# Performance work log

Hardware: AMD Instinct MI355X
Metric: run time of the kernel (lower is better)

The kernel has to match this reference:

```python
import jax, jax.numpy as jnp
import numpy as np

B, S, D = 512, 8, 1024
L = 6        # n_layers
LOOPS = 4    # n_loops
EPS = 1e-5   # LayerNorm eps (torch default)


def setup_inputs() -> dict:
    key = jax.random.key(0)
    ks = jax.random.split(key, 8)
    s = 1.0 / np.sqrt(D)  # torch Linear default init bound
    x = jax.random.normal(ks[0], (B, S, D), jnp.float32)
    gamma = jnp.ones((L, D), jnp.float32)
    beta = jnp.zeros((L, D), jnp.float32)
    Wg = jax.random.uniform(ks[1], (L, D, D), jnp.float32, -s, s)
    bg = jax.random.uniform(ks[2], (L, D), jnp.float32, -s, s)
    Wt = jax.random.uniform(ks[3], (L, D, D), jnp.float32, -s, s)
    bt = jax.random.uniform(ks[4], (L, D), jnp.float32, -s, s)
    Wc = jax.random.uniform(ks[5], (D, 1), jnp.float32, -s, s)
    bc = jax.random.uniform(ks[6], (1,), jnp.float32, -s, s)
    return {"x": x, "gamma": gamma, "beta": beta, "Wg": Wg, "bg": bg,
            "Wt": Wt, "bt": bt, "Wc": Wc, "bc": bc}


def _block(x, gamma, beta, Wg, bg, Wt, bt):
    # LayerNorm over last dim
    mu = jnp.mean(x, axis=-1, keepdims=True)
    var = jnp.mean(jnp.square(x - mu), axis=-1, keepdims=True)
    xn = (x - mu) * jax.lax.rsqrt(var + EPS) * gamma + beta
    g = jax.nn.sigmoid(jnp.einsum('bsd,de->bse', xn, Wg) + bg)
    t = jnp.tanh(jnp.einsum('bsd,de->bse', xn, Wt) + bt)
    return x * (1.0 - g) + t * g


def reference(x, gamma, beta, Wg, bg, Wt, bt, Wc, bc):
    confs = []
    for _ in range(LOOPS):
        for i in range(L):
            x = _block(x, gamma[i], beta[i], Wg[i], bg[i], Wt[i], bt[i])
        # confidence = sigmoid(Linear(x.mean(dim=1)))  -> (B, 1)
        confs.append(jax.nn.sigmoid(x.mean(axis=1) @ Wc + bc))
    return x, jnp.stack(confs)  # ((B,S,D), (LOOPS,B,1))
```

## Files before the change

### kernel.cpp

```cpp
#include <hip/hip_runtime.h>
#include <hip/hip_bf16.h>
#include <math.h>

#define B_ 512
#define S_ 8
#define D_ 1024
#define L_ 6
#define LOOPS_ 4
#define R_ (B_*S_)
#define LD_ (L_*D_)
#define EPSV 1e-5f

#define BM 128
#define BN 64
#define BK 64
#define NT (D_/BK)
#define BUF_USH 16384

typedef __attribute__((ext_vector_type(4))) float f32x4;
typedef __attribute__((ext_vector_type(8))) _Float16 f16x8;

__device__ __forceinline__ float bf2f(unsigned short u){
  union { float f; unsigned int i; } v; v.i = ((unsigned int)u) << 16; return v.f;
}
__device__ __forceinline__ unsigned short f2h(float f){
  _Float16 h = (_Float16)f;
  union { _Float16 h; unsigned short u; } v; v.h = h; return v.u;
}
__device__ __forceinline__ float loadf(const void* p, size_t i, int bf){
  return bf ? bf2f(((const unsigned short*)p)[i]) : ((const float*)p)[i];
}
__device__ __forceinline__ void gload16(const void* g, void* l){
  __builtin_amdgcn_global_load_lds((const __attribute__((address_space(1))) void*)g,
                                   (__attribute__((address_space(3))) void*)l, 16, 0, 0);
}

__global__ void k_detect(const unsigned int* __restrict__ gamma_raw, int* __restrict__ flag){
  if (threadIdx.x == 0 && blockIdx.x == 0)
    *flag = (gamma_raw[0] == 0x3F803F80u) ? 1 : 0;
}

__global__ void k_x2f(const void* __restrict__ x, float* __restrict__ xf,
                      const int* __restrict__ flag, int n4){
  int i = blockIdx.x * blockDim.x + threadIdx.x;
  if (i >= n4) return;
  if (*flag){
    ushort4 u = ((const ushort4*)x)[i];
    float4 f; f.x = bf2f(u.x); f.y = bf2f(u.y); f.z = bf2f(u.z); f.w = bf2f(u.w);
    ((float4*)xf)[i] = f;
  } else {
    ((float4*)xf)[i] = ((const float4*)x)[i];
  }
}

__global__ void k_small(const void* g, const void* b, const void* bgp, const void* btp,
                        const void* wcp, const void* bcp,
                        float* __restrict__ sm, const int* __restrict__ flag){
  int i = blockIdx.x * blockDim.x + threadIdx.x;
  int bf = *flag;
  if (i < LD_)               sm[i] = loadf(g,   i,          bf);
  else if (i < 2*LD_)        sm[i] = loadf(b,   i - LD_,    bf);
  else if (i < 3*LD_)        sm[i] = loadf(bgp, i - 2*LD_,  bf);
  else if (i < 4*LD_)        sm[i] = loadf(btp, i - 3*LD_,  bf);
  else if (i < 4*LD_ + D_)   sm[i] = loadf(wcp, i - 4*LD_,  bf);
  else if (i == 4*LD_ + D_)  sm[i] = loadf(bcp, 0,          bf);
}

__global__ void k_transpose(const void* __restrict__ Wg, const void* __restrict__ Wt,
                            ushort* __restrict__ WgT, ushort* __restrict__ WtT,
                            const int* __restrict__ flag){
  __shared__ ushort tile[32][33];
  int bf = *flag;
  int z = blockIdx.z;
  const void* src; ushort* dst;
  size_t base;
  if (z < L_) { src = Wg; dst = WgT + (size_t)z * D_ * D_;        base = (size_t)z * D_ * D_; }
  else        { src = Wt; dst = WtT + (size_t)(z - L_) * D_ * D_; base = (size_t)(z - L_) * D_ * D_; }
  int d0 = blockIdx.y * 32, e0 = blockIdx.x * 32;
  int tx = threadIdx.x, ty = threadIdx.y;
  #pragma unroll
  for (int i = 0; i < 4; i++){
    int r = ty + i * 8;
    size_t idx = base + (size_t)(d0 + r) * D_ + e0 + tx;
    float v = bf ? bf2f(((const ushort*)src)[idx]) : ((const float*)src)[idx];
    tile[r][tx] = f2h(v);
  }
  __syncthreads();
  #pragma unroll
  for (int i = 0; i < 4; i++){
    int r = ty + i * 8;
    dst[(size_t)(e0 + r) * D_ + d0 + tx] = tile[tx][r];
  }
}

__global__ __launch_bounds__(256) void k_ln(const float* __restrict__ xf,
            const float* __restrict__ gamma, const float* __restrict__ beta,
            ushort* __restrict__ xh){
  int row = blockIdx.x;
  int t = threadIdx.x;
  const float4* xr = (const float4*)(xf + (size_t)row * D_);
  float4 v = xr[t];
  float s = v.x + v.y + v.z + v.w;
  float q = v.x * v.x + v.y * v.y + v.z * v.z + v.w * v.w;
  #pragma unroll
  for (int o = 32; o; o >>= 1){ s += __shfl_xor(s, o); q += __shfl_xor(q, o); }
  __shared__ float ss[8], qq[8];
  int w = t >> 6, lane = t & 63;
  if (lane == 0){ ss[w] = s; qq[w] = q; }
  __syncthreads();
  if (t == 0){
    float S = ss[0] + ss[1] + ss[2] + ss[3];
    float Q = qq[0] + qq[1] + qq[2] + qq[3];
    float mu = S * (1.0f / D_);
    float var = Q * (1.0f / D_) - mu * mu;
    ss[4] = mu; qq[4] = rsqrtf(var + EPSV);
  }
  __syncthreads();
  float mu = ss[4], rs = qq[4];
  float4 gm4 = ((const float4*)gamma)[t];
  float4 bb4 = ((const float4*)beta)[t];
  float xv[4] = { v.x, v.y, v.z, v.w };
  float gm[4] = { gm4.x, gm4.y, gm4.z, gm4.w };
  float bb[4] = { bb4.x, bb4.y, bb4.z, bb4.w };
  ushort hu[4];
  #pragma unroll
  for (int j = 0; j < 4; j++){
    float xn = (xv[j] - mu) * rs * gm[j] + bb[j];
    hu[j] = f2h(xn);
  }
  ushort4 ho; ho.x = hu[0]; ho.y = hu[1]; ho.z = hu[2]; ho.w = hu[3];
  ((ushort4*)(xh + (size_t)row * D_))[t] = ho;
}

__device__ __forceinline__ void stage_tile(const ushort* __restrict__ xh,
    const ushort* __restrict__ wg, const ushort* __restrict__ wt,
    ushort* __restrict__ buf, int mbase, int nbase, int kb, int w, int lane)
{
  int rr = lane >> 3;
  int clog = (lane & 7) ^ rr;
  int coff = kb + clog * 8;
  #pragma unroll
  for (int i = 0; i < 4; i++){
    int row = (w * 4 + i) * 8 + rr;
    gload16(xh + (size_t)(mbase + row) * D_ + coff, buf + (w * 4 + i) * 512);
  }
  #pragma unroll
  for (int i = 0; i < 2; i++){
    int row = (w * 2 + i) * 8 + rr;
    gload16(wg + (size_t)(nbase + row) * D_ + coff, buf + 8192 + (w * 2 + i) * 512);
    gload16(wt + (size_t)(nbase + row) * D_ + coff, buf + 12288 + (w * 2 + i) * 512);
  }
}

__global__ __launch_bounds__(256, 2) void k_gemm_gate(
    const ushort* __restrict__ xh,
    const ushort* __restrict__ WgT, const ushort* __restrict__ WtT,
    const float* __restrict__ bgf, const float* __restrict__ btf,
    float* __restrict__ xf)
{
  __shared__ __align__(16) ushort smem[2 * BUF_USH];

  int t = threadIdx.x;
  int lane = t & 63, w = t >> 6;
  int wm = w >> 1, wn = w & 1;

  int bid = blockIdx.x;
  int swz = (bid & 7) * 64 + (bid >> 3);
  int mbase = (swz >> 4) * BM;
  int nbase = (swz & 15) * BN;

  f32x4 accg[4][2], acct[4][2];
  #pragma unroll
  for (int i = 0; i < 4; i++)
    #pragma unroll
    for (int j = 0; j < 2; j++){
      accg[i][j] = (f32x4){0.f, 0.f, 0.f, 0.f};
      acct[i][j] = (f32x4){0.f, 0.f, 0.f, 0.f};
    }

  ushort* b0 = smem;
  ushort* b1 = smem + BUF_USH;

  stage_tile(xh, WgT, WtT, b0, mbase, nbase, 0, w, lane);

  for (int kt = 0; kt < NT; ++kt){
    __syncthreads();
    ushort* cb = (kt & 1) ? b1 : b0;
    ushort* nbuf = (kt & 1) ? b0 : b1;
    if (kt < NT - 1)
      stage_tile(xh, WgT, WtT, nbuf, mbase, nbase, (kt + 1) * BK, w, lane);

    const ushort* bA = cb;
    const ushort* bG = cb + 8192;
    const ushort* bT = cb + 12288;
    #pragma unroll
    for (int ks = 0; ks < 2; ks++){
      int cl = ks * 4 + (lane >> 4);
      f16x8 af[4], bg2[2], bt2[2];
      #pragma unroll
      for (int mf = 0; mf < 4; mf++){
        int r = wm * 64 + mf * 16 + (lane & 15);
        af[mf] = *(const f16x8*)(bA + r * 64 + ((cl ^ (r & 7)) << 3));
      }
      #pragma unroll
      for (int nf = 0; nf < 2; nf++){
        int r = wn * 32 + nf * 16 + (lane & 15);
        int off = r * 64 + ((cl ^ (r & 7)) << 3);
        bg2[nf] = *(const f16x8*)(bG + off);
        bt2[nf] = *(const f16x8*)(bT + off);
      }
      #pragma unroll
      for (int mf = 0; mf < 4; mf++)
        #pragma unroll
        for (int nf = 0; nf < 2; nf++){
          accg[mf][nf] = __builtin_amdgcn_mfma_f32_16x16x32_f16(af[mf], bg2[nf], accg[mf][nf], 0, 0, 0);
          acct[mf][nf] = __builtin_amdgcn_mfma_f32_16x16x32_f16(af[mf], bt2[nf], acct[mf][nf], 0, 0, 0);
        }
    }
  }

  #pragma unroll
  for (int mf = 0; mf < 4; mf++){
    int row0 = mbase + wm * 64 + mf * 16 + ((lane >> 4) * 4);
    #pragma unroll
    for (int nf = 0; nf < 2; nf++){
      int col = nbase + wn * 32 + nf * 16 + (lane & 15);
      float bgv = bgf[col];
      float btv = btf[col];
      #pragma unroll
      for (int j = 0; j < 4; j++){
        float ug = accg[mf][nf][j] + bgv;
        float ut = acct[mf][nf][j] + btv;
        float g = 1.0f / (1.0f + expf(-ug));
        float tt = tanhf(ut);
        size_t idx = (size_t)(row0 + j) * D_ + col;
        float xo = xf[idx];
        xf[idx] = xo + g * (tt - xo);
      }
    }
  }
}

__global__ __launch_bounds__(256) void k_conf(const float* __restrict__ xf, const float* __restrict__ Wc,
                       const float* __restrict__ bc, float* __restrict__ out, int loop){
  int b = blockIdx.x;
  int t = threadIdx.x;
  const float* xb = xf + (size_t)b * S_ * D_;
  float acc = 0.f;
  for (int i = t; i < S_ * D_; i += 256){
    int d = i & (D_ - 1);
    acc += xb[i] * Wc[d];
  }
  #pragma unroll
  for (int o = 32; o; o >>= 1) acc += __shfl_xor(acc, o);
  __shared__ float wsum[4];
  int w = t >> 6, lane = t & 63;
  if (lane == 0) wsum[w] = acc;
  __syncthreads();
  if (t == 0){
    float s = wsum[0] + wsum[1] + wsum[2] + wsum[3];
    float z = s * (1.0f / S_) + bc[0];
    float c = 1.0f / (1.0f + expf(-z));
    out[(size_t)R_ * D_ + (size_t)loop * B_ + b] = c;
  }
}

__global__ void k_f2x(const float* __restrict__ xf, float* __restrict__ out, int n4){
  int i = blockIdx.x * blockDim.x + threadIdx.x;
  if (i >= n4) return;
  ((float4*)out)[i] = ((const float4*)xf)[i];
}

extern "C" void kernel_launch(void* const* d_in, const int* in_sizes, int n_in,
                              void* d_out, int out_size, void* d_ws, size_t ws_size,
                              hipStream_t stream){
  const void* x     = d_in[0];
  const void* gamma = d_in[1];
  const void* beta  = d_in[2];
  const void* Wg    = d_in[3];
  const void* bg    = d_in[4];
  const void* Wt    = d_in[5];
  const void* bt    = d_in[6];
  const void* Wc    = d_in[7];
  const void* bc    = d_in[8];
  float* out = (float*)d_out;

  char* ws = (char*)d_ws;
  float*  xf  = (float*)ws;
  ushort* xh  = (ushort*)(ws + (size_t)R_ * D_ * 4);
  ushort* WgT = xh + (size_t)R_ * D_;
  ushort* WtT = WgT + (size_t)L_ * D_ * D_;
  float*  sm  = (float*)(WtT + (size_t)L_ * D_ * D_);
  int*    flag = (int*)(sm + 4 * LD_ + D_ + 1);

  k_detect<<<1, 64, 0, stream>>>((const unsigned int*)gamma, flag);
  k_x2f<<<4096, 256, 0, stream>>>(x, xf, flag, R_ * D_ / 4);
  k_small<<<(4 * LD_ + D_ + 1 + 255) / 256, 256, 0, stream>>>(gamma, beta, bg, bt, Wc, bc, sm, flag);
  dim3 tb(32, 8); dim3 tg(D_ / 32, D_ / 32, 2 * L_);
  k_transpose<<<tg, tb, 0, stream>>>(Wg, Wt, WgT, WtT, flag);

  const float* smG  = sm;
  const float* smB  = sm + LD_;
  const float* smBg = sm + 2 * LD_;
  const float* smBt = sm + 3 * LD_;
  const float* smWc = sm + 4 * LD_;
  const float* smBc = sm + 4 * LD_ + D_;

  for (int loop = 0; loop < LOOPS_; ++loop){
    for (int l = 0; l < L_; ++l){
      k_ln<<<R_, 256, 0, stream>>>(xf, smG + (size_t)l * D_, smB + (size_t)l * D_, xh);
      k_gemm_gate<<<512, 256, 0, stream>>>(xh,
                                           WgT + (size_t)l * D_ * D_, WtT + (size_t)l * D_ * D_,
                                           smBg + (size_t)l * D_, smBt + (size_t)l * D_, xf);
    }
    k_conf<<<B_, 256, 0, stream>>>(xf, smWc, smBc, out, loop);
  }
  k_f2x<<<4096, 256, 0, stream>>>(xf, out, R_ * D_ / 4);
}
```

Measured before the change: 910.5 us.

## Load GEMM A operand directly to registers and use one wave per LayerNorm row

The GEMM no longer stages the activation (A) tile through LDS. Each wave loads its A fragments straight from global memory into registers, prefetched one k-step ahead, and only the two weight tiles stay in LDS. This halves LDS use and bandwidth, but raises register pressure and makes the A loads from global less coalesced. LayerNorm now handles one row per wave with four rows per block, which removes the shared-memory reductions and barriers.

```diff
diff --git a/kernel.cpp b/kernel.cpp
--- a/kernel.cpp
+++ b/kernel.cpp
@@ -15,7 +15,7 @@
 #define BN 64
 #define BK 64
 #define NT (D_/BK)
-#define BUF_USH 16384
+#define BUF_USH 8192
 
 typedef __attribute__((ext_vector_type(4))) float f32x4;
 typedef __attribute__((ext_vector_type(8))) _Float16 f16x8;
@@ -96,60 +96,60 @@
 __global__ __launch_bounds__(256) void k_ln(const float* __restrict__ xf,
             const float* __restrict__ gamma, const float* __restrict__ beta,
             ushort* __restrict__ xh){
-  int row = blockIdx.x;
-  int t = threadIdx.x;
-  const float4* xr = (const float4*)(xf + (size_t)row * D_);
-  float4 v = xr[t];
-  float s = v.x + v.y + v.z + v.w;
-  float q = v.x * v.x + v.y * v.y + v.z * v.z + v.w * v.w;
+  int w = threadIdx.x >> 6, lane = threadIdx.x & 63;
+  int row = blockIdx.x * 4 + w;
+  const float* xr = xf + (size_t)row * D_;
+  float4 v[4];
+  float s = 0.f, q = 0.f;
+  #pragma unroll
+  for (int p = 0; p < 4; p++){
+    v[p] = *(const float4*)(xr + p * 256 + lane * 4);
+    s += v[p].x + v[p].y + v[p].z + v[p].w;
+    q += v[p].x * v[p].x + v[p].y * v[p].y + v[p].z * v[p].z + v[p].w * v[p].w;
+  }
   #pragma unroll
   for (int o = 32; o; o >>= 1){ s += __shfl_xor(s, o); q += __shfl_xor(q, o); }
-  __shared__ float ss[8], qq[8];
-  int w = t >> 6, lane = t & 63;
-  if (lane == 0){ ss[w] = s; qq[w] = q; }
-  __syncthreads();
-  if (t == 0){
-    float S = ss[0] + ss[1] + ss[2] + ss[3];
-    float Q = qq[0] + qq[1] + qq[2] + qq[3];
-    float mu = S * (1.0f / D_);
-    float var = Q * (1.0f / D_) - mu * mu;
-    ss[4] = mu; qq[4] = rsqrtf(var + EPSV);
-  }
-  __syncthreads();
-  float mu = ss[4], rs = qq[4];
-  float4 gm4 = ((const float4*)gamma)[t];
-  float4 bb4 = ((const float4*)beta)[t];
-  float xv[4] = { v.x, v.y, v.z, v.w };
-  float gm[4] = { gm4.x, gm4.y, gm4.z, gm4.w };
-  float bb[4] = { bb4.x, bb4.y, bb4.z, bb4.w };
-  ushort hu[4];
-  #pragma unroll
-  for (int j = 0; j < 4; j++){
-    float xn = (xv[j] - mu) * rs * gm[j] + bb[j];
-    hu[j] = f2h(xn);
-  }
-  ushort4 ho; ho.x = hu[0]; ho.y = hu[1]; ho.z = hu[2]; ho.w = hu[3];
-  ((ushort4*)(xh + (size_t)row * D_))[t] = ho;
-}
-
-__device__ __forceinline__ void stage_tile(const ushort* __restrict__ xh,
-    const ushort* __restrict__ wg, const ushort* __restrict__ wt,
-    ushort* __restrict__ buf, int mbase, int nbase, int kb, int w, int lane)
+  float mu = s * (1.0f / D_);
+  float var = q * (1.0f / D_) - mu * mu;
+  float rs = rsqrtf(var + EPSV);
+  #pragma unroll
+  for (int p = 0; p < 4; p++){
+    float4 g4 = *(const float4*)(gamma + p * 256 + lane * 4);
+    float4 b4 = *(const float4*)(beta  + p * 256 + lane * 4);
+    ushort4 o4;
+    o4.x = f2h((v[p].x - mu) * rs * g4.x + b4.x);
+    o4.y = f2h((v[p].y - mu) * rs * g4.y + b4.y);
+    o4.z = f2h((v[p].z - mu) * rs * g4.z + b4.z);
+    o4.w = f2h((v[p].w - mu) * rs * g4.w + b4.w);
+    *(ushort4*)(xh + (size_t)row * D_ + p * 256 + lane * 4) = o4;
+  }
+}
+
+__device__ __forceinline__ void stage_B(const ushort* __restrict__ wg,
+    const ushort* __restrict__ wt, ushort* __restrict__ buf,
+    int nbase, int kb, int w, int lane)
 {
   int rr = lane >> 3;
   int clog = (lane & 7) ^ rr;
   int coff = kb + clog * 8;
   #pragma unroll
-  for (int i = 0; i < 4; i++){
-    int row = (w * 4 + i) * 8 + rr;
-    gload16(xh + (size_t)(mbase + row) * D_ + coff, buf + (w * 4 + i) * 512);
-  }
-  #pragma unroll
   for (int i = 0; i < 2; i++){
     int row = (w * 2 + i) * 8 + rr;
-    gload16(wg + (size_t)(nbase + row) * D_ + coff, buf + 8192 + (w * 2 + i) * 512);
-    gload16(wt + (size_t)(nbase + row) * D_ + coff, buf + 12288 + (w * 2 + i) * 512);
-  }
+    gload16(wg + (size_t)(nbase + row) * D_ + coff, buf + (w * 2 + i) * 512);
+    gload16(wt + (size_t)(nbase + row) * D_ + coff, buf + 4096 + (w * 2 + i) * 512);
+  }
+}
+
+__device__ __forceinline__ void load_A(const ushort* __restrict__ xh,
+    f16x8* af, int mbase, int wm, int lane, int kb)
+{
+  #pragma unroll
+  for (int ks = 0; ks < 2; ks++)
+    #pragma unroll
+    for (int mf = 0; mf < 4; mf++){
+      int r = mbase + wm * 64 + mf * 16 + (lane & 15);
+      af[ks * 4 + mf] = *(const f16x8*)(xh + (size_t)r * D_ + kb + ks * 32 + (lane >> 4) * 8);
+    }
 }
 
 __global__ __launch_bounds__(256, 2) void k_gemm_gate(
@@ -181,27 +181,25 @@
   ushort* b0 = smem;
   ushort* b1 = smem + BUF_USH;
 
-  stage_tile(xh, WgT, WtT, b0, mbase, nbase, 0, w, lane);
+  f16x8 afc[8], afn[8];
+  stage_B(WgT, WtT, b0, nbase, 0, w, lane);
+  load_A(xh, afc, mbase, wm, lane, 0);
 
   for (int kt = 0; kt < NT; ++kt){
     __syncthreads();
     ushort* cb = (kt & 1) ? b1 : b0;
     ushort* nbuf = (kt & 1) ? b0 : b1;
-    if (kt < NT - 1)
-      stage_tile(xh, WgT, WtT, nbuf, mbase, nbase, (kt + 1) * BK, w, lane);
-
-    const ushort* bA = cb;
-    const ushort* bG = cb + 8192;
-    const ushort* bT = cb + 12288;
+    if (kt < NT - 1){
+      stage_B(WgT, WtT, nbuf, nbase, (kt + 1) * BK, w, lane);
+      load_A(xh, afn, mbase, wm, lane, (kt + 1) * BK);
+    }
+
+    const ushort* bG = cb;
+    const ushort* bT = cb + 4096;
     #pragma unroll
     for (int ks = 0; ks < 2; ks++){
       int cl = ks * 4 + (lane >> 4);
-      f16x8 af[4], bg2[2], bt2[2];
-      #pragma unroll
-      for (int mf = 0; mf < 4; mf++){
-        int r = wm * 64 + mf * 16 + (lane & 15);
-        af[mf] = *(const f16x8*)(bA + r * 64 + ((cl ^ (r & 7)) << 3));
-      }
+      f16x8 bg2[2], bt2[2];
       #pragma unroll
       for (int nf = 0; nf < 2; nf++){
         int r = wn * 32 + nf * 16 + (lane & 15);
@@ -213,10 +211,12 @@
       for (int mf = 0; mf < 4; mf++)
         #pragma unroll
         for (int nf = 0; nf < 2; nf++){
-          accg[mf][nf] = __builtin_amdgcn_mfma_f32_16x16x32_f16(af[mf], bg2[nf], accg[mf][nf], 0, 0, 0);
-          acct[mf][nf] = __builtin_amdgcn_mfma_f32_16x16x32_f16(af[mf], bt2[nf], acct[mf][nf], 0, 0, 0);
+          accg[mf][nf] = __builtin_amdgcn_mfma_f32_16x16x32_f16(afc[ks * 4 + mf], bg2[nf], accg[mf][nf], 0, 0, 0);
+          acct[mf][nf] = __builtin_amdgcn_mfma_f32_16x16x32_f16(afc[ks * 4 + mf], bt2[nf], acct[mf][nf], 0, 0, 0);
         }
     }
+    #pragma unroll
+    for (int i = 0; i < 8; i++) afc[i] = afn[i];
   }
 
   #pragma unroll
@@ -308,7 +308,7 @@
 
   for (int loop = 0; loop < LOOPS_; ++loop){
     for (int l = 0; l < L_; ++l){
-      k_ln<<<R_, 256, 0, stream>>>(xf, smG + (size_t)l * D_, smB + (size_t)l * D_, xh);
+      k_ln<<<R_ / 4, 256, 0, stream>>>(xf, smG + (size_t)l * D_, smB + (size_t)l * D_, xh);
       k_gemm_gate<<<512, 256, 0, stream>>>(xh,
                                            WgT + (size_t)l * D_ * D_, WtT + (size_t)l * D_ * D_,
                                            smBg + (size_t)l * D_, smBt + (size_t)l * D_, xf);
```

After: 1.344 ms (median of 5 runs). +47.7%, slower.
